# Kernel tuning notes

Measured on AMD Instinct MI355X. Metric: run time of the kernel, lower is better.

The kernel has to match this reference:

```python
import jax, jax.numpy as jnp
import numpy as np

B, C, H, W = 16, 512, 32, 32
EPS = 1e-5

def setup_inputs() -> dict:
    key = jax.random.key(0)
    ks = jax.random.split(key, 7)
    s = 1.0 / np.sqrt(C)
    return {
        "x": jax.random.normal(ks[0], (B, C, H, W), dtype=jnp.float32),
        "norm_w": jnp.ones((C,), jnp.float32),
        "norm_b": jnp.zeros((C,), jnp.float32),
        "qkv_w": jax.random.normal(ks[1], (3 * C, C), dtype=jnp.float32) * s,
        "qkv_b": jax.random.normal(ks[2], (3 * C,), dtype=jnp.float32) * 0.01,
        "out_w": jax.random.normal(ks[3], (C, C), dtype=jnp.float32) * s,
        "out_b": jax.random.normal(ks[4], (C,), dtype=jnp.float32) * 0.01,
    }

def reference(x, norm_w, norm_b, qkv_w, qkv_b, out_w, out_b):
    b, c, h, w = x.shape
    # GroupNorm with num_groups=1: normalize over (C,H,W) per sample, per-channel affine
    mean = jnp.mean(x, axis=(1, 2, 3), keepdims=True)
    var = jnp.var(x, axis=(1, 2, 3), keepdims=True)
    xn = (x - mean) * jax.lax.rsqrt(var + EPS)
    xn = xn * norm_w[None, :, None, None] + norm_b[None, :, None, None]
    # 1x1 conv QKV: [b,3c,h,w]
    qkv = jnp.einsum('bchw,oc->bohw', xn, qkv_w) + qkv_b[None, :, None, None]
    q, k, v = jnp.split(qkv, 3, axis=1)
    n = h * w
    q = q.transpose(0, 2, 3, 1).reshape(b, n, c)   # [b, N, c]
    k = k.reshape(b, c, n)                          # [b, c, N]
    v = v.transpose(0, 2, 3, 1).reshape(b, n, c)   # [b, N, c]
    scores = jnp.einsum('bnc,bcm->bnm', q, k) * (c ** -0.5)  # [b, N, N]
    attn = jax.nn.softmax(scores, axis=-1)
    out = jnp.einsum('bnm,bmc->bnc', attn, v)       # [b, N, c]
    out = out.reshape(b, h, w, c).transpose(0, 3, 1, 2)
    out = jnp.einsum('bchw,oc->bohw', out, out_w) + out_b[None, :, None, None]
    return out + x
```

## Files before the change

### kernel.cpp

```cpp
#include <hip/hip_runtime.h>
#include <math.h>

#define BATCH 16
#define CH    512
#define NTOK  1024
#define CHW   (CH * NTOK)
#define EPSV  1e-5f

typedef __attribute__((ext_vector_type(8))) short bf16x8;
typedef __attribute__((ext_vector_type(4))) float f32x4;

__device__ __forceinline__ unsigned short f2bf(float f) {
    union { float f; unsigned u; } cv; cv.f = f;
    unsigned r = cv.u + 0x7FFFu + ((cv.u >> 16) & 1u);
    return (unsigned short)(r >> 16);
}
__device__ __forceinline__ float bf2f(unsigned short u) {
    union { unsigned u; float f; } cv; cv.u = ((unsigned)u) << 16;
    return cv.f;
}

__device__ __forceinline__ void async16(const unsigned short* g, unsigned short* l) {
    __builtin_amdgcn_global_load_lds(
        (const __attribute__((address_space(1))) void*)g,
        (__attribute__((address_space(3))) void*)l,
        16, 0, 0);
}

static const size_t OFF_WQKV = 256;
static const size_t OFF_OW   = OFF_WQKV + 1572864;
static const size_t OFF_XNT  = OFF_OW   + 524288;
static const size_t OFF_QT   = OFF_XNT  + 16777216;
static const size_t OFF_KT   = OFF_QT   + 16777216;
static const size_t OFF_V    = OFF_KT   + 16777216;
static const size_t OFF_OT   = OFF_V    + 16777216;
static const size_t OFF_S    = OFF_OT   + 16777216;
static const size_t OFF_P    = OFF_S    + 33554432;

__global__ void k_zero_stats(float* ws) {
    if (threadIdx.x < 64) ws[threadIdx.x] = 0.0f;
}

__global__ __launch_bounds__(256) void k_stats_partial(const float* __restrict__ x, float* __restrict__ ws) {
    int blk   = blockIdx.x;
    int b     = blk >> 6;
    int chunk = blk & 63;
    const float4* xp = (const float4*)(x + (size_t)b * CHW + (size_t)chunk * 8192);
    int t = threadIdx.x;
    float s = 0.0f, ss = 0.0f;
#pragma unroll
    for (int j = 0; j < 8; j++) {
        float4 v = xp[t + j * 256];
        s  += v.x + v.y + v.z + v.w;
        ss += v.x * v.x + v.y * v.y + v.z * v.z + v.w * v.w;
    }
#pragma unroll
    for (int off = 32; off; off >>= 1) {
        s  += __shfl_xor(s, off, 64);
        ss += __shfl_xor(ss, off, 64);
    }
    __shared__ float ls[4], lss[4];
    int wave = t >> 6, lane = t & 63;
    if (lane == 0) { ls[wave] = s; lss[wave] = ss; }
    __syncthreads();
    if (t == 0) {
        atomicAdd(&ws[b], ls[0] + ls[1] + ls[2] + ls[3]);
        atomicAdd(&ws[16 + b], lss[0] + lss[1] + lss[2] + lss[3]);
    }
}

__global__ void k_stats_final(float* ws) {
    int b = threadIdx.x;
    if (b < 16) {
        float inv  = 1.0f / (float)CHW;
        float mean = ws[b] * inv;
        float var  = ws[16 + b] * inv - mean * mean;
        ws[32 + b] = mean;
        ws[48 + b] = rsqrtf(var + EPSV);
    }
}

__global__ __launch_bounds__(256) void k_cvt(const float* __restrict__ in, unsigned short* __restrict__ out, int n4) {
    int i = blockIdx.x * 256 + threadIdx.x;
    if (i < n4) {
        float4 v = ((const float4*)in)[i];
        ushort4 o;
        o.x = f2bf(v.x); o.y = f2bf(v.y); o.z = f2bf(v.z); o.w = f2bf(v.w);
        ((ushort4*)out)[i] = o;
    }
}

__global__ __launch_bounds__(256) void k_xnt(const float* __restrict__ x,
                                             const float* __restrict__ nw,
                                             const float* __restrict__ nb,
                                             const float* __restrict__ ws,
                                             unsigned short* __restrict__ xnt) {
    __shared__ float ls[64][65];
    int b  = blockIdx.z;
    int c0 = blockIdx.y * 64;
    int n0 = blockIdx.x * 64;
    float mean = ws[32 + b], rstd = ws[48 + b];
    int t = threadIdx.x;
    int cl = t >> 4, n4 = t & 15;
    const float* xb = x + (size_t)b * CHW;
#pragma unroll
    for (int i = 0; i < 4; i++) {
        int c = c0 + cl + i * 16;
        float a  = rstd * nw[c];
        float bb = nb[c] - mean * a;
        float4 v = *(const float4*)(xb + (size_t)c * NTOK + n0 + n4 * 4);
        ls[cl + i * 16][n4 * 4 + 0] = v.x * a + bb;
        ls[cl + i * 16][n4 * 4 + 1] = v.y * a + bb;
        ls[cl + i * 16][n4 * 4 + 2] = v.z * a + bb;
        ls[cl + i * 16][n4 * 4 + 3] = v.w * a + bb;
    }
    __syncthreads();
    int nl = t >> 4, c4 = t & 15;
    unsigned short* dst = xnt + (size_t)b * NTOK * CH;
#pragma unroll
    for (int i = 0; i < 4; i++) {
        int n = n0 + nl + i * 16;
        ushort4 o;
        o.x = f2bf(ls[c4 * 4 + 0][nl + i * 16]);
        o.y = f2bf(ls[c4 * 4 + 1][nl + i * 16]);
        o.z = f2bf(ls[c4 * 4 + 2][nl + i * 16]);
        o.w = f2bf(ls[c4 * 4 + 3][nl + i * 16]);
        *(ushort4*)(dst + (size_t)n * CH + c0 + c4 * 4) = o;
    }
}

__device__ __forceinline__ void mfma_core(const unsigned short* __restrict__ A, int lda,
                                          const unsigned short* __restrict__ B, int ldb,
                                          int K, int m0, int n0,
                                          unsigned short* sm,
                                          f32x4 acc[4][4]) {
    const int t = threadIdx.x;
    const int w = t >> 6, lane = t & 63;
    const int wm = (w & 1) * 64, wn = (w >> 1) * 64;
    const int r16 = lane & 15, quad = lane >> 4;
#pragma unroll
    for (int i = 0; i < 4; i++)
#pragma unroll
        for (int j = 0; j < 4; j++) acc[i][j] = (f32x4){0.f, 0.f, 0.f, 0.f};
    const int sr = lane >> 2;
    const int sk = (lane & 3) * 8;
    const unsigned short* gA0 = A + (size_t)(m0 + w * 32 + sr) * lda + sk;
    const unsigned short* gA1 = gA0 + (size_t)16 * lda;
    const unsigned short* gB0 = B + (size_t)(n0 + w * 32 + sr) * ldb + sk;
    const unsigned short* gB1 = gB0 + (size_t)16 * ldb;
    unsigned short* lA0 = sm + (w * 32) * 32;
    unsigned short* lA1 = sm + (w * 32 + 16) * 32;
    unsigned short* lB0 = sm + 8192 + (w * 32) * 32;
    unsigned short* lB1 = sm + 8192 + (w * 32 + 16) * 32;
    const int T = K >> 5;
    async16(gA0, lA0);
    async16(gA1, lA1);
    async16(gB0, lB0);
    async16(gB1, lB1);
    for (int tt = 0; tt < T; tt++) {
        __syncthreads();
        const int cur = (tt & 1) << 12;
        if (tt + 1 < T) {
            const int nxt = cur ^ 4096;
            const int ko = (tt + 1) << 5;
            async16(gA0 + ko, lA0 + nxt);
            async16(gA1 + ko, lA1 + nxt);
            async16(gB0 + ko, lB0 + nxt);
            async16(gB1 + ko, lB1 + nxt);
        }
        bf16x8 af[4], bfr[4];
#pragma unroll
        for (int i = 0; i < 4; i++) af[i]  = *(const bf16x8*)(sm + cur + (wm + i * 16 + r16) * 32 + quad * 8);
#pragma unroll
        for (int j = 0; j < 4; j++) bfr[j] = *(const bf16x8*)(sm + 8192 + cur + (wn + j * 16 + r16) * 32 + quad * 8);
#pragma unroll
        for (int i = 0; i < 4; i++)
#pragma unroll
            for (int j = 0; j < 4; j++)
                acc[i][j] = __builtin_amdgcn_mfma_f32_16x16x32_bf16(af[i], bfr[j], acc[i][j], 0, 0, 0);
    }
}

#define TSTRIDE 136

__global__ __launch_bounds__(256) void k_gemm_qkv(const unsigned short* __restrict__ Wq,
                                                  const float* __restrict__ qb,
                                                  const unsigned short* __restrict__ XNT,
                                                  unsigned short* __restrict__ QT,
                                                  unsigned short* __restrict__ KT,
                                                  unsigned short* __restrict__ V) {
    __shared__ __align__(16) unsigned short smem[128 * TSTRIDE];
    const int b  = blockIdx.z;
    const int m0 = blockIdx.y * 128;
    const int n0 = blockIdx.x * 128;
    f32x4 acc[4][4];
    mfma_core(Wq, CH, XNT + (size_t)b * NTOK * CH, CH, CH, m0, n0, smem, acc);
    const int t = threadIdx.x;
    const int w = t >> 6, lane = t & 63;
    const int wm = (w & 1) * 64, wn = (w >> 1) * 64;
    const int r16 = lane & 15, quad = lane >> 4;
    const int region = m0 >> 9;
    __syncthreads();
    if (region < 2) {
#pragma unroll
        for (int i = 0; i < 4; i++) {
            const int ol = wm + i * 16 + quad * 4;
            const int og = m0 + ol;
            const float b0 = qb[og], b1 = qb[og + 1], b2 = qb[og + 2], b3 = qb[og + 3];
#pragma unroll
            for (int j = 0; j < 4; j++) {
                const int nl = wn + j * 16 + r16;
                f32x4 a = acc[i][j];
                ushort4 pk;
                pk.x = f2bf(a[0] + b0); pk.y = f2bf(a[1] + b1);
                pk.z = f2bf(a[2] + b2); pk.w = f2bf(a[3] + b3);
                *(ushort4*)(smem + nl * TSTRIDE + ol) = pk;
            }
        }
        __syncthreads();
        unsigned short* dst = ((region == 0) ? QT : KT) + (size_t)b * NTOK * CH + (size_t)n0 * CH + (m0 & 511);
#pragma unroll
        for (int p = 0; p < 16; p++) {
            const int row = (t >> 5) + p * 8;
            const int seg = (t & 31) * 4;
            *(ushort4*)(dst + (size_t)row * CH + seg) = *(const ushort4*)(smem + row * TSTRIDE + seg);
        }
    } else {
#pragma unroll
        for (int i = 0; i < 4; i++) {
            const int ol = wm + i * 16 + quad * 4;
            const int og = m0 + ol;
#pragma unroll
            for (int j = 0; j < 4; j++) {
                const int nl = wn + j * 16 + r16;
                f32x4 a = acc[i][j];
#pragma unroll
                for (int r = 0; r < 4; r++)
                    smem[(ol + r) * TSTRIDE + nl] = f2bf(a[r] + qb[og + r]);
            }
        }
        __syncthreads();
        unsigned short* dst = V + (size_t)b * CH * NTOK + (size_t)(m0 & 511) * NTOK + n0;
#pragma unroll
        for (int p = 0; p < 16; p++) {
            const int row = (t >> 5) + p * 8;
            const int seg = (t & 31) * 4;
            *(ushort4*)(dst + (size_t)row * NTOK + seg) = *(const ushort4*)(smem + row * TSTRIDE + seg);
        }
    }
}

__global__ __launch_bounds__(256) void k_gemm_sc(const unsigned short* __restrict__ QT,
                                                 const unsigned short* __restrict__ KT,
                                                 unsigned short* __restrict__ S) {
    __shared__ __align__(16) unsigned short smem[16384];
    const int b  = blockIdx.z;
    const int m0 = blockIdx.y * 128;
    const int n0 = blockIdx.x * 128;
    f32x4 acc[4][4];
    mfma_core(QT + (size_t)b * NTOK * CH, CH, KT + (size_t)b * NTOK * CH, CH, CH, m0, n0, smem, acc);
    const int t = threadIdx.x;
    const int w = t >> 6, lane = t & 63;
    const int wm = (w & 1) * 64, wn = (w >> 1) * 64;
    const int r16 = lane & 15, quad = lane >> 4;
    const float scale = 0.044194173824159216f;
    unsigned short* Sb = S + (size_t)b * NTOK * NTOK;
#pragma unroll
    for (int i = 0; i < 4; i++) {
        const int row0 = m0 + wm + i * 16 + quad * 4;
#pragma unroll
        for (int j = 0; j < 4; j++) {
            const int col = n0 + wn + j * 16 + r16;
            f32x4 a = acc[i][j];
#pragma unroll
            for (int r = 0; r < 4; r++)
                Sb[(size_t)(row0 + r) * NTOK + col] = f2bf(a[r] * scale);
        }
    }
}

__global__ __launch_bounds__(256) void k_softmax(const unsigned short* __restrict__ S, unsigned short* __restrict__ P) {
    size_t row = blockIdx.x;
    const unsigned short* p = S + row * NTOK;
    unsigned short* q = P + row * NTOK;
    int t = threadIdx.x;
    int wave = t >> 6, lane = t & 63;
    __shared__ float red[4];
    ushort4 u = ((const ushort4*)p)[t];
    float4 v;
    v.x = bf2f(u.x); v.y = bf2f(u.y); v.z = bf2f(u.z); v.w = bf2f(u.w);
    float m = fmaxf(fmaxf(v.x, v.y), fmaxf(v.z, v.w));
#pragma unroll
    for (int off = 32; off; off >>= 1) m = fmaxf(m, __shfl_xor(m, off, 64));
    if (lane == 0) red[wave] = m;
    __syncthreads();
    m = fmaxf(fmaxf(red[0], red[1]), fmaxf(red[2], red[3]));
    __syncthreads();
    v.x = __expf(v.x - m);
    v.y = __expf(v.y - m);
    v.z = __expf(v.z - m);
    v.w = __expf(v.w - m);
    float s = v.x + v.y + v.z + v.w;
#pragma unroll
    for (int off = 32; off; off >>= 1) s += __shfl_xor(s, off, 64);
    if (lane == 0) red[wave] = s;
    __syncthreads();
    s = red[0] + red[1] + red[2] + red[3];
    float inv = 1.0f / s;
    ushort4 o;
    o.x = f2bf(v.x * inv); o.y = f2bf(v.y * inv); o.z = f2bf(v.z * inv); o.w = f2bf(v.w * inv);
    ((ushort4*)q)[t] = o;
}

__global__ __launch_bounds__(256) void k_gemm_av(const unsigned short* __restrict__ V,
                                                 const unsigned short* __restrict__ P,
                                                 unsigned short* __restrict__ OT) {
    __shared__ __align__(16) unsigned short smem[128 * TSTRIDE];
    const int b  = blockIdx.z;
    const int m0 = blockIdx.y * 128;
    const int n0 = blockIdx.x * 128;
    f32x4 acc[4][4];
    mfma_core(V + (size_t)b * CH * NTOK, NTOK, P + (size_t)b * NTOK * NTOK, NTOK, NTOK, m0, n0, smem, acc);
    const int t = threadIdx.x;
    const int w = t >> 6, lane = t & 63;
    const int wm = (w & 1) * 64, wn = (w >> 1) * 64;
    const int r16 = lane & 15, quad = lane >> 4;
    __syncthreads();
#pragma unroll
    for (int i = 0; i < 4; i++) {
        const int cl = wm + i * 16 + quad * 4;
#pragma unroll
        for (int j = 0; j < 4; j++) {
            const int nl = wn + j * 16 + r16;
            f32x4 a = acc[i][j];
            ushort4 pk;
            pk.x = f2bf(a[0]); pk.y = f2bf(a[1]); pk.z = f2bf(a[2]); pk.w = f2bf(a[3]);
            *(ushort4*)(smem + nl * TSTRIDE + cl) = pk;
        }
    }
    __syncthreads();
    unsigned short* dst = OT + (size_t)b * NTOK * CH + (size_t)n0 * CH + m0;
#pragma unroll
    for (int p = 0; p < 16; p++) {
        const int row = (t >> 5) + p * 8;
        const int seg = (t & 31) * 4;
        *(ushort4*)(dst + (size_t)row * CH + seg) = *(const ushort4*)(smem + row * TSTRIDE + seg);
    }
}

__global__ __launch_bounds__(256) void k_gemm_out(const unsigned short* __restrict__ OW,
                                                  const float* __restrict__ ob,
                                                  const unsigned short* __restrict__ OT,
                                                  const float* __restrict__ x,
                                                  float* __restrict__ out) {
    __shared__ __align__(16) unsigned short smem[16384];
    const int b  = blockIdx.z;
    const int m0 = blockIdx.y * 128;
    const int n0 = blockIdx.x * 128;
    f32x4 acc[4][4];
    mfma_core(OW, CH, OT + (size_t)b * NTOK * CH, CH, CH, m0, n0, smem, acc);
    const int t = threadIdx.x;
    const int w = t >> 6, lane = t & 63;
    const int wm = (w & 1) * 64, wn = (w >> 1) * 64;
    const int r16 = lane & 15, quad = lane >> 4;
#pragma unroll
    for (int i = 0; i < 4; i++) {
        const int o0g = m0 + wm + i * 16 + quad * 4;
#pragma unroll
        for (int j = 0; j < 4; j++) {
            const int col = n0 + wn + j * 16 + r16;
            f32x4 a = acc[i][j];
#pragma unroll
            for (int r = 0; r < 4; r++) {
                size_t idx = (size_t)b * CHW + (size_t)(o0g + r) * NTOK + col;
                out[idx] = a[r] + ob[o0g + r] + x[idx];
            }
        }
    }
}

extern "C" void kernel_launch(void* const* d_in, const int* in_sizes, int n_in,
                              void* d_out, int out_size, void* d_ws, size_t ws_size,
                              hipStream_t stream) {
    const float* x      = (const float*)d_in[0];
    const float* norm_w = (const float*)d_in[1];
    const float* norm_b = (const float*)d_in[2];
    const float* qkv_w  = (const float*)d_in[3];
    const float* qkv_b  = (const float*)d_in[4];
    const float* out_w  = (const float*)d_in[5];
    const float* out_b  = (const float*)d_in[6];
    float* out = (float*)d_out;
    char* wsb  = (char*)d_ws;

    float* stats = (float*)wsb;
    unsigned short* WQ  = (unsigned short*)(wsb + OFF_WQKV);
    unsigned short* OW  = (unsigned short*)(wsb + OFF_OW);
    unsigned short* XNT = (unsigned short*)(wsb + OFF_XNT);
    unsigned short* QT  = (unsigned short*)(wsb + OFF_QT);
    unsigned short* KT  = (unsigned short*)(wsb + OFF_KT);
    unsigned short* V   = (unsigned short*)(wsb + OFF_V);
    unsigned short* OT  = (unsigned short*)(wsb + OFF_OT);
    unsigned short* S   = (unsigned short*)(wsb + OFF_S);
    unsigned short* P   = (unsigned short*)(wsb + OFF_P);

    k_zero_stats<<<1, 64, 0, stream>>>(stats);
    k_stats_partial<<<BATCH * 64, 256, 0, stream>>>(x, stats);
    k_stats_final<<<1, 16, 0, stream>>>(stats);
    k_cvt<<<768, 256, 0, stream>>>(qkv_w, WQ, 3 * CH * CH / 4);
    k_cvt<<<256, 256, 0, stream>>>(out_w, OW, CH * CH / 4);
    k_xnt<<<dim3(NTOK / 64, CH / 64, BATCH), 256, 0, stream>>>(x, norm_w, norm_b, stats, XNT);
    k_gemm_qkv<<<dim3(NTOK / 128, 3 * CH / 128, BATCH), 256, 0, stream>>>(WQ, qkv_b, XNT, QT, KT, V);
    k_gemm_sc<<<dim3(NTOK / 128, NTOK / 128, BATCH), 256, 0, stream>>>(QT, KT, S);
    k_softmax<<<BATCH * NTOK, 256, 0, stream>>>(S, P);
    k_gemm_av<<<dim3(NTOK / 128, CH / 128, BATCH), 256, 0, stream>>>(V, P, OT);
    k_gemm_out<<<dim3(NTOK / 128, CH / 128, BATCH), 256, 0, stream>>>(OW, out_b, OT, x, out);
}
```

Before: 258.6 us.

## Widen GEMM tiles to 128x256, stage score output through LDS, merge weight converts

Every bf16 MFMA GEMM now uses a 128x256 block tile, so each wave holds a 64x128 accumulator and issues twice as many B loads and MFMAs per K step. This raises arithmetic intensity per block and halves the grid size, at the cost of more registers and LDS per block. launch_bounds is set to request 2 blocks per CU. The score GEMM now stages its bf16 output through LDS so it can write coalesced 8-byte rows instead of scattered 2-byte stores, and the two weight-conversion launches are merged into one kernel.

```diff
diff --git a/kernel.cpp b/kernel.cpp
--- a/kernel.cpp
+++ b/kernel.cpp
@@ -80,14 +80,16 @@
     }
 }
 
-__global__ __launch_bounds__(256) void k_cvt(const float* __restrict__ in, unsigned short* __restrict__ out, int n4) {
+__global__ __launch_bounds__(256) void k_cvt2(const float* __restrict__ wq, const float* __restrict__ wo,
+                                              unsigned short* __restrict__ WQ, unsigned short* __restrict__ WO) {
     int i = blockIdx.x * 256 + threadIdx.x;
-    if (i < n4) {
-        float4 v = ((const float4*)in)[i];
-        ushort4 o;
-        o.x = f2bf(v.x); o.y = f2bf(v.y); o.z = f2bf(v.z); o.w = f2bf(v.w);
-        ((ushort4*)out)[i] = o;
-    }
+    const float* src; unsigned short* dst; int off;
+    if (i < 196608) { src = wq; dst = WQ; off = i; }
+    else            { src = wo; dst = WO; off = i - 196608; }
+    float4 v = ((const float4*)src)[off];
+    ushort4 o;
+    o.x = f2bf(v.x); o.y = f2bf(v.y); o.z = f2bf(v.z); o.w = f2bf(v.w);
+    ((ushort4*)dst)[off] = o;
 }
 
 __global__ __launch_bounds__(256) void k_xnt(const float* __restrict__ x,
@@ -129,75 +131,78 @@
     }
 }
 
-__device__ __forceinline__ void mfma_core(const unsigned short* __restrict__ A, int lda,
-                                          const unsigned short* __restrict__ B, int ldb,
-                                          int K, int m0, int n0,
-                                          unsigned short* sm,
-                                          f32x4 acc[4][4]) {
+__device__ __forceinline__ void mfma_core2(const unsigned short* __restrict__ A, int lda,
+                                           const unsigned short* __restrict__ B, int ldb,
+                                           int K, int m0, int n0,
+                                           unsigned short* sm,
+                                           f32x4 acc[4][8]) {
     const int t = threadIdx.x;
     const int w = t >> 6, lane = t & 63;
-    const int wm = (w & 1) * 64, wn = (w >> 1) * 64;
+    const int wm = (w & 1) * 64, wn = (w >> 1) * 128;
     const int r16 = lane & 15, quad = lane >> 4;
 #pragma unroll
     for (int i = 0; i < 4; i++)
 #pragma unroll
-        for (int j = 0; j < 4; j++) acc[i][j] = (f32x4){0.f, 0.f, 0.f, 0.f};
+        for (int j = 0; j < 8; j++) acc[i][j] = (f32x4){0.f, 0.f, 0.f, 0.f};
     const int sr = lane >> 2;
     const int sk = (lane & 3) * 8;
     const unsigned short* gA0 = A + (size_t)(m0 + w * 32 + sr) * lda + sk;
     const unsigned short* gA1 = gA0 + (size_t)16 * lda;
-    const unsigned short* gB0 = B + (size_t)(n0 + w * 32 + sr) * ldb + sk;
+    const unsigned short* gB0 = B + (size_t)(n0 + w * 64 + sr) * ldb + sk;
     const unsigned short* gB1 = gB0 + (size_t)16 * ldb;
+    const unsigned short* gB2 = gB0 + (size_t)32 * ldb;
+    const unsigned short* gB3 = gB0 + (size_t)48 * ldb;
     unsigned short* lA0 = sm + (w * 32) * 32;
     unsigned short* lA1 = sm + (w * 32 + 16) * 32;
-    unsigned short* lB0 = sm + 8192 + (w * 32) * 32;
-    unsigned short* lB1 = sm + 8192 + (w * 32 + 16) * 32;
+    unsigned short* lB0 = sm + 8192 + (w * 64) * 32;
+    unsigned short* lB1 = lB0 + 16 * 32;
+    unsigned short* lB2 = lB0 + 32 * 32;
+    unsigned short* lB3 = lB0 + 48 * 32;
     const int T = K >> 5;
-    async16(gA0, lA0);
-    async16(gA1, lA1);
-    async16(gB0, lB0);
-    async16(gB1, lB1);
+    async16(gA0, lA0); async16(gA1, lA1);
+    async16(gB0, lB0); async16(gB1, lB1); async16(gB2, lB2); async16(gB3, lB3);
     for (int tt = 0; tt < T; tt++) {
         __syncthreads();
-        const int cur = (tt & 1) << 12;
+        const int ab = (tt & 1) << 12;
+        const int bb = (tt & 1) << 13;
         if (tt + 1 < T) {
-            const int nxt = cur ^ 4096;
+            const int nab = ab ^ 4096, nbb = bb ^ 8192;
             const int ko = (tt + 1) << 5;
-            async16(gA0 + ko, lA0 + nxt);
-            async16(gA1 + ko, lA1 + nxt);
-            async16(gB0 + ko, lB0 + nxt);
-            async16(gB1 + ko, lB1 + nxt);
-        }
-        bf16x8 af[4], bfr[4];
-#pragma unroll
-        for (int i = 0; i < 4; i++) af[i]  = *(const bf16x8*)(sm + cur + (wm + i * 16 + r16) * 32 + quad * 8);
-#pragma unroll
-        for (int j = 0; j < 4; j++) bfr[j] = *(const bf16x8*)(sm + 8192 + cur + (wn + j * 16 + r16) * 32 + quad * 8);
+            async16(gA0 + ko, lA0 + nab); async16(gA1 + ko, lA1 + nab);
+            async16(gB0 + ko, lB0 + nbb); async16(gB1 + ko, lB1 + nbb);
+            async16(gB2 + ko, lB2 + nbb); async16(gB3 + ko, lB3 + nbb);
+        }
+        bf16x8 af[4], bfr[8];
+#pragma unroll
+        for (int i = 0; i < 4; i++) af[i]  = *(const bf16x8*)(sm + ab + (wm + i * 16 + r16) * 32 + quad * 8);
+#pragma unroll
+        for (int j = 0; j < 8; j++) bfr[j] = *(const bf16x8*)(sm + 8192 + bb + (wn + j * 16 + r16) * 32 + quad * 8);
 #pragma unroll
         for (int i = 0; i < 4; i++)
 #pragma unroll
-            for (int j = 0; j < 4; j++)
+            for (int j = 0; j < 8; j++)
                 acc[i][j] = __builtin_amdgcn_mfma_f32_16x16x32_bf16(af[i], bfr[j], acc[i][j], 0, 0, 0);
     }
 }
 
-#define TSTRIDE 136
-
-__global__ __launch_bounds__(256) void k_gemm_qkv(const unsigned short* __restrict__ Wq,
-                                                  const float* __restrict__ qb,
-                                                  const unsigned short* __restrict__ XNT,
-                                                  unsigned short* __restrict__ QT,
-                                                  unsigned short* __restrict__ KT,
-                                                  unsigned short* __restrict__ V) {
-    __shared__ __align__(16) unsigned short smem[128 * TSTRIDE];
+#define TS1 136
+#define TS2 264
+
+__global__ __launch_bounds__(256, 2) void k_gemm_qkv(const unsigned short* __restrict__ Wq,
+                                                     const float* __restrict__ qb,
+                                                     const unsigned short* __restrict__ XNT,
+                                                     unsigned short* __restrict__ QT,
+                                                     unsigned short* __restrict__ KT,
+                                                     unsigned short* __restrict__ V) {
+    __shared__ __align__(16) unsigned short smem[256 * TS1];
     const int b  = blockIdx.z;
     const int m0 = blockIdx.y * 128;
-    const int n0 = blockIdx.x * 128;
-    f32x4 acc[4][4];
-    mfma_core(Wq, CH, XNT + (size_t)b * NTOK * CH, CH, CH, m0, n0, smem, acc);
+    const int n0 = blockIdx.x * 256;
+    f32x4 acc[4][8];
+    mfma_core2(Wq, CH, XNT + (size_t)b * NTOK * CH, CH, CH, m0, n0, smem, acc);
     const int t = threadIdx.x;
     const int w = t >> 6, lane = t & 63;
-    const int wm = (w & 1) * 64, wn = (w >> 1) * 64;
+    const int wm = (w & 1) * 64, wn = (w >> 1) * 128;
     const int r16 = lane & 15, quad = lane >> 4;
     const int region = m0 >> 9;
     __syncthreads();
@@ -208,22 +213,22 @@
             const int og = m0 + ol;
             const float b0 = qb[og], b1 = qb[og + 1], b2 = qb[og + 2], b3 = qb[og + 3];
 #pragma unroll
-            for (int j = 0; j < 4; j++) {
+            for (int j = 0; j < 8; j++) {
                 const int nl = wn + j * 16 + r16;
                 f32x4 a = acc[i][j];
                 ushort4 pk;
                 pk.x = f2bf(a[0] + b0); pk.y = f2bf(a[1] + b1);
                 pk.z = f2bf(a[2] + b2); pk.w = f2bf(a[3] + b3);
-                *(ushort4*)(smem + nl * TSTRIDE + ol) = pk;
+                *(ushort4*)(smem + nl * TS1 + ol) = pk;
             }
         }
         __syncthreads();
         unsigned short* dst = ((region == 0) ? QT : KT) + (size_t)b * NTOK * CH + (size_t)n0 * CH + (m0 & 511);
 #pragma unroll
-        for (int p = 0; p < 16; p++) {
+        for (int p = 0; p < 32; p++) {
             const int row = (t >> 5) + p * 8;
             const int seg = (t & 31) * 4;
-            *(ushort4*)(dst + (size_t)row * CH + seg) = *(const ushort4*)(smem + row * TSTRIDE + seg);
+            *(ushort4*)(dst + (size_t)row * CH + seg) = *(const ushort4*)(smem + row * TS1 + seg);
         }
     } else {
 #pragma unroll
@@ -231,51 +236,59 @@
             const int ol = wm + i * 16 + quad * 4;
             const int og = m0 + ol;
 #pragma unroll
-            for (int j = 0; j < 4; j++) {
+            for (int j = 0; j < 8; j++) {
                 const int nl = wn + j * 16 + r16;
                 f32x4 a = acc[i][j];
 #pragma unroll
                 for (int r = 0; r < 4; r++)
-                    smem[(ol + r) * TSTRIDE + nl] = f2bf(a[r] + qb[og + r]);
+                    smem[(ol + r) * TS2 + nl] = f2bf(a[r] + qb[og + r]);
             }
         }
         __syncthreads();
         unsigned short* dst = V + (size_t)b * CH * NTOK + (size_t)(m0 & 511) * NTOK + n0;
 #pragma unroll
-        for (int p = 0; p < 16; p++) {
-            const int row = (t >> 5) + p * 8;
-            const int seg = (t & 31) * 4;
-            *(ushort4*)(dst + (size_t)row * NTOK + seg) = *(const ushort4*)(smem + row * TSTRIDE + seg);
-        }
-    }
-}
-
-__global__ __launch_bounds__(256) void k_gemm_sc(const unsigned short* __restrict__ QT,
-                                                 const unsigned short* __restrict__ KT,
-                                                 unsigned short* __restrict__ S) {
-    __shared__ __align__(16) unsigned short smem[16384];
+        for (int p = 0; p < 32; p++) {
+            const int row = (t >> 5) + (p & 15) * 8;
+            const int seg = (t & 31) * 4 + (p >> 4) * 128;
+            *(ushort4*)(dst + (size_t)row * NTOK + seg) = *(const ushort4*)(smem + row * TS2 + seg);
+        }
+    }
+}
+
+__global__ __launch_bounds__(256, 2) void k_gemm_sc(const unsigned short* __restrict__ QT,
+                                                    const unsigned short* __restrict__ KT,
+                                                    unsigned short* __restrict__ S) {
+    __shared__ __align__(16) unsigned short smem[256 * TS1];
     const int b  = blockIdx.z;
     const int m0 = blockIdx.y * 128;
-    const int n0 = blockIdx.x * 128;
-    f32x4 acc[4][4];
-    mfma_core(QT + (size_t)b * NTOK * CH, CH, KT + (size_t)b * NTOK * CH, CH, CH, m0, n0, smem, acc);
+    const int n0 = blockIdx.x * 256;
+    f32x4 acc[4][8];
+    mfma_core2(QT + (size_t)b * NTOK * CH, CH, KT + (size_t)b * NTOK * CH, CH, CH, m0, n0, smem, acc);
     const int t = threadIdx.x;
     const int w = t >> 6, lane = t & 63;
-    const int wm = (w & 1) * 64, wn = (w >> 1) * 64;
+    const int wm = (w & 1) * 64, wn = (w >> 1) * 128;
     const int r16 = lane & 15, quad = lane >> 4;
     const float scale = 0.044194173824159216f;
-    unsigned short* Sb = S + (size_t)b * NTOK * NTOK;
+    __syncthreads();
 #pragma unroll
     for (int i = 0; i < 4; i++) {
-        const int row0 = m0 + wm + i * 16 + quad * 4;
-#pragma unroll
-        for (int j = 0; j < 4; j++) {
-            const int col = n0 + wn + j * 16 + r16;
+        const int ml = wm + i * 16 + quad * 4;
+#pragma unroll
+        for (int j = 0; j < 8; j++) {
+            const int kl = wn + j * 16 + r16;
             f32x4 a = acc[i][j];
 #pragma unroll
             for (int r = 0; r < 4; r++)
-                Sb[(size_t)(row0 + r) * NTOK + col] = f2bf(a[r] * scale);
-        }
+                smem[(ml + r) * TS2 + kl] = f2bf(a[r] * scale);
+        }
+    }
+    __syncthreads();
+    unsigned short* dst = S + (size_t)b * NTOK * NTOK + (size_t)m0 * NTOK + n0;
+#pragma unroll
+    for (int p = 0; p < 32; p++) {
+        const int row = (t >> 5) + (p & 15) * 8;
+        const int seg = (t & 31) * 4 + (p >> 4) * 128;
+        *(ushort4*)(dst + (size_t)row * NTOK + seg) = *(const ushort4*)(smem + row * TS2 + seg);
     }
 }
 
@@ -312,62 +325,62 @@
     ((ushort4*)q)[t] = o;
 }
 
-__global__ __launch_bounds__(256) void k_gemm_av(const unsigned short* __restrict__ V,
-                                                 const unsigned short* __restrict__ P,
-                                                 unsigned short* __restrict__ OT) {
-    __shared__ __align__(16) unsigned short smem[128 * TSTRIDE];
+__global__ __launch_bounds__(256, 2) void k_gemm_av(const unsigned short* __restrict__ V,
+                                                    const unsigned short* __restrict__ P,
+                                                    unsigned short* __restrict__ OT) {
+    __shared__ __align__(16) unsigned short smem[256 * TS1];
     const int b  = blockIdx.z;
     const int m0 = blockIdx.y * 128;
-    const int n0 = blockIdx.x * 128;
-    f32x4 acc[4][4];
-    mfma_core(V + (size_t)b * CH * NTOK, NTOK, P + (size_t)b * NTOK * NTOK, NTOK, NTOK, m0, n0, smem, acc);
+    const int n0 = blockIdx.x * 256;
+    f32x4 acc[4][8];
+    mfma_core2(V + (size_t)b * CH * NTOK, NTOK, P + (size_t)b * NTOK * NTOK, NTOK, NTOK, m0, n0, smem, acc);
     const int t = threadIdx.x;
     const int w = t >> 6, lane = t & 63;
-    const int wm = (w & 1) * 64, wn = (w >> 1) * 64;
+    const int wm = (w & 1) * 64, wn = (w >> 1) * 128;
     const int r16 = lane & 15, quad = lane >> 4;
     __syncthreads();
 #pragma unroll
     for (int i = 0; i < 4; i++) {
         const int cl = wm + i * 16 + quad * 4;
 #pragma unroll
-        for (int j = 0; j < 4; j++) {
+        for (int j = 0; j < 8; j++) {
             const int nl = wn + j * 16 + r16;
             f32x4 a = acc[i][j];
             ushort4 pk;
             pk.x = f2bf(a[0]); pk.y = f2bf(a[1]); pk.z = f2bf(a[2]); pk.w = f2bf(a[3]);
-            *(ushort4*)(smem + nl * TSTRIDE + cl) = pk;
+            *(ushort4*)(smem + nl * TS1 + cl) = pk;
         }
     }
     __syncthreads();
     unsigned short* dst = OT + (size_t)b * NTOK * CH + (size_t)n0 * CH + m0;
 #pragma unroll
-    for (int p = 0; p < 16; p++) {
+    for (int p = 0; p < 32; p++) {
         const int row = (t >> 5) + p * 8;
         const int seg = (t & 31) * 4;
-        *(ushort4*)(dst + (size_t)row * CH + seg) = *(const ushort4*)(smem + row * TSTRIDE + seg);
-    }
-}
-
-__global__ __launch_bounds__(256) void k_gemm_out(const unsigned short* __restrict__ OW,
-                                                  const float* __restrict__ ob,
-                                                  const unsigned short* __restrict__ OT,
-                                                  const float* __restrict__ x,
-                                                  float* __restrict__ out) {
-    __shared__ __align__(16) unsigned short smem[16384];
+        *(ushort4*)(dst + (size_t)row * CH + seg) = *(const ushort4*)(smem + row * TS1 + seg);
+    }
+}
+
+__global__ __launch_bounds__(256, 2) void k_gemm_out(const unsigned short* __restrict__ OW,
+                                                     const float* __restrict__ ob,
+                                                     const unsigned short* __restrict__ OT,
+                                                     const float* __restrict__ x,
+                                                     float* __restrict__ out) {
+    __shared__ __align__(16) unsigned short smem[24576];
     const int b  = blockIdx.z;
     const int m0 = blockIdx.y * 128;
-    const int n0 = blockIdx.x * 128;
-    f32x4 acc[4][4];
-    mfma_core(OW, CH, OT + (size_t)b * NTOK * CH, CH, CH, m0, n0, smem, acc);
+    const int n0 = blockIdx.x * 256;
+    f32x4 acc[4][8];
+    mfma_core2(OW, CH, OT + (size_t)b * NTOK * CH, CH, CH, m0, n0, smem, acc);
     const int t = threadIdx.x;
     const int w = t >> 6, lane = t & 63;
-    const int wm = (w & 1) * 64, wn = (w >> 1) * 64;
+    const int wm = (w & 1) * 64, wn = (w >> 1) * 128;
     const int r16 = lane & 15, quad = lane >> 4;
 #pragma unroll
     for (int i = 0; i < 4; i++) {
         const int o0g = m0 + wm + i * 16 + quad * 4;
 #pragma unroll
-        for (int j = 0; j < 4; j++) {
+        for (int j = 0; j < 8; j++) {
             const int col = n0 + wn + j * 16 + r16;
             f32x4 a = acc[i][j];
 #pragma unroll
@@ -406,12 +419,11 @@
     k_zero_stats<<<1, 64, 0, stream>>>(stats);
     k_stats_partial<<<BATCH * 64, 256, 0, stream>>>(x, stats);
     k_stats_final<<<1, 16, 0, stream>>>(stats);
-    k_cvt<<<768, 256, 0, stream>>>(qkv_w, WQ, 3 * CH * CH / 4);
-    k_cvt<<<256, 256, 0, stream>>>(out_w, OW, CH * CH / 4);
+    k_cvt2<<<1024, 256, 0, stream>>>(qkv_w, out_w, WQ, OW);
     k_xnt<<<dim3(NTOK / 64, CH / 64, BATCH), 256, 0, stream>>>(x, norm_w, norm_b, stats, XNT);
-    k_gemm_qkv<<<dim3(NTOK / 128, 3 * CH / 128, BATCH), 256, 0, stream>>>(WQ, qkv_b, XNT, QT, KT, V);
-    k_gemm_sc<<<dim3(NTOK / 128, NTOK / 128, BATCH), 256, 0, stream>>>(QT, KT, S);
+    k_gemm_qkv<<<dim3(NTOK / 256, 3 * CH / 128, BATCH), 256, 0, stream>>>(WQ, qkv_b, XNT, QT, KT, V);
+    k_gemm_sc<<<dim3(NTOK / 256, NTOK / 128, BATCH), 256, 0, stream>>>(QT, KT, S);
     k_softmax<<<BATCH * NTOK, 256, 0, stream>>>(S, P);
-    k_gemm_av<<<dim3(NTOK / 128, CH / 128, BATCH), 256, 0, stream>>>(V, P, OT);
-    k_gemm_out<<<dim3(NTOK / 128, CH / 128, BATCH), 256, 0, stream>>>(OW, out_b, OT, x, out);
-}
+    k_gemm_av<<<dim3(NTOK / 256, CH / 128, BATCH), 256, 0, stream>>>(V, P, OT);
+    k_gemm_out<<<dim3(NTOK / 256, CH / 128, BATCH), 256, 0, stream>>>(OW, out_b, OT, x, out);
+}
```

Result: faster. 245.6 us (-5.0%).
